# Kernel tuning notes

Measured on AMD Instinct MI355X. Metric: run time of the kernel, lower is better.

Reference implementation:

```python
import jax, jax.numpy as jnp
import numpy as np

H = 1.0  # RBF bandwidth (init kwarg h)


def setup_inputs() -> dict:
    key = jax.random.key(0)
    k1, k2 = jax.random.split(key)
    x = jax.random.normal(k1, (8192, 512), dtype=jnp.float32)
    x1 = jax.random.normal(k2, (8192, 512), dtype=jnp.float32)
    return {"x": x, "x1": x1}


def reference(x, x1):
    # exp(-||x_i - x1_j||^2 / h), computed via the GEMM trick to avoid the
    # O(N*M*D) broadcast intermediate the original torch code materializes.
    x_sq = jnp.sum(x * x, axis=-1, keepdims=True)          # [N, 1]
    x1_sq = jnp.sum(x1 * x1, axis=-1)                       # [M]
    cross = jnp.einsum('nd,md->nm', x, x1)                  # [N, M]
    d = jnp.maximum(x_sq + x1_sq[None, :] - 2.0 * cross, 0.0)
    return jnp.exp(-d / H)
```

## Files before the change

### kernel.cpp

```cpp
#include <hip/hip_runtime.h>
#include <stdint.h>
#include <stddef.h>


#define NROWS 8192
#define DIMK  512
#define BM    128
#define BN    128
#define BKB   128
#define KT    (DIMK / BKB)

typedef __bf16 bf16x8 __attribute__((ext_vector_type(8)));
typedef int    i32x8  __attribute__((ext_vector_type(8)));
typedef float  f32x4  __attribute__((ext_vector_type(4)));

#define AS1 __attribute__((address_space(1)))
#define AS3 __attribute__((address_space(3)))

__device__ __forceinline__ uint32_t f2bf(float f) {
    uint32_t u = __float_as_uint(f);
    return (u + 0x7FFFu + ((u >> 16) & 1u)) >> 16;
}

__device__ __forceinline__ uint32_t pk_fp8x4(float a, float b, float c, float d) {
    int w = __builtin_amdgcn_cvt_pk_fp8_f32(a, b, 0, false);
    w     = __builtin_amdgcn_cvt_pk_fp8_f32(c, d, w, true);
    return (uint32_t)w;
}

__global__ __launch_bounds__(256) void precast_fp8(
    const float* __restrict__ x, const float* __restrict__ x1,
    uint8_t* __restrict__ xf, uint8_t* __restrict__ x1f,
    float* __restrict__ xsq, float* __restrict__ x1sq)
{
    const int w    = threadIdx.x >> 6;
    const int lane = threadIdx.x & 63;
    const int row  = blockIdx.x * 4 + w;
    const float* src;
    uint8_t* dstb;
    float* dsts;
    if (blockIdx.y == 0) { src = x  + (size_t)row * DIMK; dstb = xf  + (size_t)row * DIMK; dsts = xsq  + row; }
    else                 { src = x1 + (size_t)row * DIMK; dstb = x1f + (size_t)row * DIMK; dsts = x1sq + row; }

    float4 v0 = ((const float4*)src)[lane * 2];
    float4 v1 = ((const float4*)src)[lane * 2 + 1];
    float s = v0.x * v0.x + v0.y * v0.y + v0.z * v0.z + v0.w * v0.w
            + v1.x * v1.x + v1.y * v1.y + v1.z * v1.z + v1.w * v1.w;

    uint2 p;
    p.x = pk_fp8x4(v0.x, v0.y, v0.z, v0.w);
    p.y = pk_fp8x4(v1.x, v1.y, v1.z, v1.w);
    ((uint2*)dstb)[lane] = p;

    #pragma unroll
    for (int off = 32; off > 0; off >>= 1) s += __shfl_down(s, off);
    if (lane == 0) *dsts = s;
}

__global__ __launch_bounds__(256) void norms_only(
    const float* __restrict__ x, const float* __restrict__ x1,
    float* __restrict__ xsq, float* __restrict__ x1sq)
{
    const int row = blockIdx.x;
    const float* src = (blockIdx.y == 0) ? x + (size_t)row * DIMK : x1 + (size_t)row * DIMK;
    float* dsts      = (blockIdx.y == 0) ? xsq + row : x1sq + row;
    const int t = threadIdx.x;
    float2 v = ((const float2*)src)[t];
    float s = v.x * v.x + v.y * v.y;
    #pragma unroll
    for (int off = 32; off > 0; off >>= 1) s += __shfl_down(s, off);
    __shared__ float red[4];
    if ((t & 63) == 0) red[t >> 6] = s;
    __syncthreads();
    if (t == 0) *dsts = red[0] + red[1] + red[2] + red[3];
}

__global__ __launch_bounds__(256, 3) void rbf_mfma_mxfp8(
    const uint8_t* __restrict__ Xf, const uint8_t* __restrict__ X1f,
    const float* __restrict__ xsq, const float* __restrict__ x1sq,
    float* __restrict__ out)
{
    __shared__ uint8_t As[BM * BKB];
    __shared__ uint8_t Bs[BN * BKB];

    const int t    = threadIdx.x;
    const int bm   = blockIdx.x;
    const int bn   = blockIdx.y;
    const int lane = t & 63;
    const int w    = t >> 6;
    const int wm   = w >> 1;
    const int wn   = w & 1;

    const int srow = t >> 3;
    const int scol = (t & 7) * 16;
    const uint8_t* gA = Xf  + (size_t)(bm * BM + srow) * DIMK + scol;
    const uint8_t* gB = X1f + (size_t)(bn * BN + srow) * DIMK + scol;
    uint8_t* lA = &As[t * 16];
    uint8_t* lB = &Bs[t * 16];

    f32x4 acc[4][4];
    #pragma unroll
    for (int i = 0; i < 4; ++i)
        #pragma unroll
        for (int j = 0; j < 4; ++j)
            acc[i][j] = f32x4{0.f, 0.f, 0.f, 0.f};

    const int lrow = lane & 15;
    const int kq   = (lane >> 4) * 32;
    int aoff[4], boff[4];
    #pragma unroll
    for (int i = 0; i < 4; ++i) {
        aoff[i] = (wm * 64 + i * 16 + lrow) * BKB + kq;
        boff[i] = (wn * 64 + i * 16 + lrow) * BKB + kq;
    }

    #pragma unroll 1
    for (int kt = 0; kt < KT; ++kt) {
        const uint8_t* ga = gA + kt * BKB;
        const uint8_t* gb = gB + kt * BKB;
        #pragma unroll
        for (int c = 0; c < 4; ++c) {
            __builtin_amdgcn_global_load_lds((AS1 void*)(ga + (size_t)c * 32 * DIMK),
                                             (AS3 void*)(lA + c * 4096), 16, 0, 0);
            __builtin_amdgcn_global_load_lds((AS1 void*)(gb + (size_t)c * 32 * DIMK),
                                             (AS3 void*)(lB + c * 4096), 16, 0, 0);
        }
        __syncthreads();

        i32x8 af[4], bg[4];
        #pragma unroll
        for (int i = 0; i < 4; ++i) af[i] = *(const i32x8*)&As[aoff[i]];
        #pragma unroll
        for (int i = 0; i < 4; ++i) bg[i] = *(const i32x8*)&Bs[boff[i]];
        #pragma unroll
        for (int i = 0; i < 4; ++i)
            #pragma unroll
            for (int j = 0; j < 4; ++j)
                acc[i][j] = __builtin_amdgcn_mfma_scale_f32_16x16x128_f8f6f4(
                    af[i], bg[j], acc[i][j],
                    0, 0,
                    0, 0x7F7F7F7F,
                    0, 0x7F7F7F7F);
        if (kt + 1 < KT) __syncthreads();
    }

    const int row0 = bm * BM + wm * 64 + (lane >> 4) * 4;
    const int col0 = bn * BN + wn * 64 + lrow;
    float xs[4][4], x1s[4];
    #pragma unroll
    for (int tm = 0; tm < 4; ++tm)
        #pragma unroll
        for (int r = 0; r < 4; ++r) xs[tm][r] = xsq[row0 + tm * 16 + r];
    #pragma unroll
    for (int tn = 0; tn < 4; ++tn) x1s[tn] = x1sq[col0 + tn * 16];

    #pragma unroll
    for (int tm = 0; tm < 4; ++tm)
        #pragma unroll
        for (int tn = 0; tn < 4; ++tn)
            #pragma unroll
            for (int r = 0; r < 4; ++r) {
                const int row = row0 + tm * 16 + r;
                const int col = col0 + tn * 16;
                float d = xs[tm][r] + x1s[tn] - 2.0f * acc[tm][tn][r];
                d = fmaxf(d, 0.0f);
                __builtin_nontemporal_store(__expf(-d), &out[(size_t)row * NROWS + col]);
            }
}

__global__ __launch_bounds__(256) void rbf_mfma_inline(
    const float* __restrict__ X, const float* __restrict__ X1,
    const float* __restrict__ xsq, const float* __restrict__ x1sq,
    float* __restrict__ out)
{
    __shared__ uint16_t As[BM * 32];
    __shared__ uint16_t Bs[BN * 32];

    const int t    = threadIdx.x;
    const int bm   = blockIdx.x;
    const int bn   = blockIdx.y;
    const int lane = t & 63;
    const int w    = t >> 6;
    const int wm   = w >> 1;
    const int wn   = w & 1;

    f32x4 acc[4][4];
    #pragma unroll
    for (int i = 0; i < 4; ++i)
        #pragma unroll
        for (int j = 0; j < 4; ++j)
            acc[i][j] = f32x4{0.f, 0.f, 0.f, 0.f};

    const int lrow = lane & 15;
    const int kq   = (lane >> 4) * 8;
    int aoff[4], boff[4];
    #pragma unroll
    for (int i = 0; i < 4; ++i) {
        aoff[i] = (wm * 64 + i * 16 + lrow) * 32 + kq;
        boff[i] = (wn * 64 + i * 16 + lrow) * 32 + kq;
    }

    #pragma unroll 1
    for (int kt = 0; kt < DIMK / 32; ++kt) {
        #pragma unroll
        for (int i = 0; i < 4; ++i) {
            const int g   = t + i * 256;
            const int row = g >> 3;
            const int c4  = (g & 7) * 4;
            float4 va = *(const float4*)&X [(size_t)(bm * BM + row) * DIMK + kt * 32 + c4];
            float4 vb = *(const float4*)&X1[(size_t)(bn * BN + row) * DIMK + kt * 32 + c4];
            uint2 pa, pb;
            pa.x = f2bf(va.x) | (f2bf(va.y) << 16);
            pa.y = f2bf(va.z) | (f2bf(va.w) << 16);
            pb.x = f2bf(vb.x) | (f2bf(vb.y) << 16);
            pb.y = f2bf(vb.z) | (f2bf(vb.w) << 16);
            *(uint2*)&As[g * 4] = pa;
            *(uint2*)&Bs[g * 4] = pb;
        }
        __syncthreads();

        bf16x8 af[4], bg[4];
        #pragma unroll
        for (int i = 0; i < 4; ++i) af[i] = *(const bf16x8*)&As[aoff[i]];
        #pragma unroll
        for (int i = 0; i < 4; ++i) bg[i] = *(const bf16x8*)&Bs[boff[i]];
        #pragma unroll
        for (int i = 0; i < 4; ++i)
            #pragma unroll
            for (int j = 0; j < 4; ++j)
                acc[i][j] = __builtin_amdgcn_mfma_f32_16x16x32_bf16(af[i], bg[j], acc[i][j], 0, 0, 0);
        __syncthreads();
    }

    const int row0 = bm * BM + wm * 64 + (lane >> 4) * 4;
    const int col0 = bn * BN + wn * 64 + lrow;
    float xs[4][4], x1s[4];
    #pragma unroll
    for (int tm = 0; tm < 4; ++tm)
        #pragma unroll
        for (int r = 0; r < 4; ++r) xs[tm][r] = xsq[row0 + tm * 16 + r];
    #pragma unroll
    for (int tn = 0; tn < 4; ++tn) x1s[tn] = x1sq[col0 + tn * 16];

    #pragma unroll
    for (int tm = 0; tm < 4; ++tm)
        #pragma unroll
        for (int tn = 0; tn < 4; ++tn)
            #pragma unroll
            for (int r = 0; r < 4; ++r) {
                const int row = row0 + tm * 16 + r;
                const int col = col0 + tn * 16;
                float d = xs[tm][r] + x1s[tn] - 2.0f * acc[tm][tn][r];
                d = fmaxf(d, 0.0f);
                out[(size_t)row * NROWS + col] = __expf(-d);
            }
}

extern "C" void kernel_launch(void* const* d_in, const int* in_sizes, int n_in,
                              void* d_out, int out_size, void* d_ws, size_t ws_size,
                              hipStream_t stream)
{
    const float* x  = (const float*)d_in[0];
    const float* x1 = (const float*)d_in[1];
    float* out = (float*)d_out;

    const size_t f8_bytes  = (size_t)NROWS * DIMK;
    const size_t need_full = 2 * f8_bytes + 2 * (size_t)NROWS * sizeof(float);

    dim3 gridG(NROWS / BM, NROWS / BN);

    if (ws_size >= need_full) {
        uint8_t* xf   = (uint8_t*)d_ws;
        uint8_t* x1f  = xf + f8_bytes;
        float*   xsq  = (float*)((char*)d_ws + 2 * f8_bytes);
        float*   x1sq = xsq + NROWS;
        precast_fp8<<<dim3(NROWS / 4, 2), 256, 0, stream>>>(x, x1, xf, x1f, xsq, x1sq);
        rbf_mfma_mxfp8<<<gridG, 256, 0, stream>>>(xf, x1f, xsq, x1sq, out);
    } else {
        float* xsq  = (float*)d_ws;
        float* x1sq = xsq + NROWS;
        norms_only<<<dim3(NROWS, 2), 256, 0, stream>>>(x, x1, xsq, x1sq);
        rbf_mfma_inline<<<gridG, 256, 0, stream>>>(x, x1, xsq, x1sq, out);
    }
}
```

Baseline: 319.2 us.

## Swizzle LDS layout for fp8 MFMA tiles and hoist norm loads

Applies an XOR swizzle to the 16-byte chunks written into shared memory and reads fragments through two matching 16-byte loads, to reduce LDS bank conflicts on the MFMA operand reads. It also moves the squared-norm loads before the main loop so they overlap with the GEMM, fully unrolls the K loop, and drops the occupancy hint from the launch bounds. Output stores change from nontemporal to plain stores, which may affect cache behaviour on the large 256MB output write.

```diff
diff --git a/kernel.cpp b/kernel.cpp
--- a/kernel.cpp
+++ b/kernel.cpp
@@ -12,6 +12,7 @@
 
 typedef __bf16 bf16x8 __attribute__((ext_vector_type(8)));
 typedef int    i32x8  __attribute__((ext_vector_type(8)));
+typedef int    i32x4  __attribute__((ext_vector_type(4)));
 typedef float  f32x4  __attribute__((ext_vector_type(4)));
 
 #define AS1 __attribute__((address_space(1)))
@@ -26,6 +27,15 @@
     int w = __builtin_amdgcn_cvt_pk_fp8_f32(a, b, 0, false);
     w     = __builtin_amdgcn_cvt_pk_fp8_f32(c, d, w, true);
     return (uint32_t)w;
+}
+
+__device__ __forceinline__ i32x8 ld_frag(const uint8_t* base, int c_lo, int c_hi) {
+    i32x4 lo = *(const i32x4*)(base + c_lo);
+    i32x4 hi = *(const i32x4*)(base + c_hi);
+    i32x8 r;
+    r[0] = lo[0]; r[1] = lo[1]; r[2] = lo[2]; r[3] = lo[3];
+    r[4] = hi[0]; r[5] = hi[1]; r[6] = hi[2]; r[7] = hi[3];
+    return r;
 }
 
 __global__ __launch_bounds__(256) void precast_fp8(
@@ -75,7 +85,7 @@
     if (t == 0) *dsts = red[0] + red[1] + red[2] + red[3];
 }
 
-__global__ __launch_bounds__(256, 3) void rbf_mfma_mxfp8(
+__global__ __launch_bounds__(256) void rbf_mfma_mxfp8(
     const uint8_t* __restrict__ Xf, const uint8_t* __restrict__ X1f,
     const float* __restrict__ xsq, const float* __restrict__ x1sq,
     float* __restrict__ out)
@@ -91,13 +101,24 @@
     const int wm   = w >> 1;
     const int wn   = w & 1;
 
-    const int srow = t >> 3;
-    const int scol = (t & 7) * 16;
-    const uint8_t* gA = Xf  + (size_t)(bm * BM + srow) * DIMK + scol;
-    const uint8_t* gB = X1f + (size_t)(bn * BN + srow) * DIMK + scol;
+    const int srow   = t >> 3;
+    const int schunk = (t & 7) ^ (srow & 7);
+    const uint8_t* gA = Xf  + (size_t)(bm * BM + srow) * DIMK + schunk * 16;
+    const uint8_t* gB = X1f + (size_t)(bn * BN + srow) * DIMK + schunk * 16;
     uint8_t* lA = &As[t * 16];
     uint8_t* lB = &Bs[t * 16];
 
+    const int lrow = lane & 15;
+    const int row0 = bm * BM + wm * 64 + (lane >> 4) * 4;
+    const int col0 = bn * BN + wn * 64 + lrow;
+    float xs[4][4], x1s[4];
+    #pragma unroll
+    for (int tm = 0; tm < 4; ++tm)
+        #pragma unroll
+        for (int r = 0; r < 4; ++r) xs[tm][r] = xsq[row0 + tm * 16 + r];
+    #pragma unroll
+    for (int tn = 0; tn < 4; ++tn) x1s[tn] = x1sq[col0 + tn * 16];
+
     f32x4 acc[4][4];
     #pragma unroll
     for (int i = 0; i < 4; ++i)
@@ -105,16 +126,15 @@
         for (int j = 0; j < 4; ++j)
             acc[i][j] = f32x4{0.f, 0.f, 0.f, 0.f};
 
-    const int lrow = lane & 15;
-    const int kq   = (lane >> 4) * 32;
-    int aoff[4], boff[4];
-    #pragma unroll
-    for (int i = 0; i < 4; ++i) {
-        aoff[i] = (wm * 64 + i * 16 + lrow) * BKB + kq;
-        boff[i] = (wn * 64 + i * 16 + lrow) * BKB + kq;
-    }
-
-    #pragma unroll 1
+    const int q    = lane >> 4;
+    const int s    = lrow & 7;
+    const int c_lo = ((2 * q)     ^ s) * 16;
+    const int c_hi = ((2 * q + 1) ^ s) * 16;
+    int roff[4];
+    #pragma unroll
+    for (int i = 0; i < 4; ++i) roff[i] = (i * 16 + lrow) * BKB;
+
+    #pragma unroll
     for (int kt = 0; kt < KT; ++kt) {
         const uint8_t* ga = gA + kt * BKB;
         const uint8_t* gb = gB + kt * BKB;
@@ -129,9 +149,11 @@
 
         i32x8 af[4], bg[4];
         #pragma unroll
-        for (int i = 0; i < 4; ++i) af[i] = *(const i32x8*)&As[aoff[i]];
-        #pragma unroll
-        for (int i = 0; i < 4; ++i) bg[i] = *(const i32x8*)&Bs[boff[i]];
+        for (int i = 0; i < 4; ++i)
+            af[i] = ld_frag(&As[wm * 64 * BKB + roff[i]], c_lo, c_hi);
+        #pragma unroll
+        for (int i = 0; i < 4; ++i)
+            bg[i] = ld_frag(&Bs[wn * 64 * BKB + roff[i]], c_lo, c_hi);
         #pragma unroll
         for (int i = 0; i < 4; ++i)
             #pragma unroll
@@ -141,18 +163,8 @@
                     0, 0,
                     0, 0x7F7F7F7F,
                     0, 0x7F7F7F7F);
-        if (kt + 1 < KT) __syncthreads();
-    }
-
-    const int row0 = bm * BM + wm * 64 + (lane >> 4) * 4;
-    const int col0 = bn * BN + wn * 64 + lrow;
-    float xs[4][4], x1s[4];
-    #pragma unroll
-    for (int tm = 0; tm < 4; ++tm)
-        #pragma unroll
-        for (int r = 0; r < 4; ++r) xs[tm][r] = xsq[row0 + tm * 16 + r];
-    #pragma unroll
-    for (int tn = 0; tn < 4; ++tn) x1s[tn] = x1sq[col0 + tn * 16];
+        __syncthreads();
+    }
 
     #pragma unroll
     for (int tm = 0; tm < 4; ++tm)
@@ -164,7 +176,7 @@
                 const int col = col0 + tn * 16;
                 float d = xs[tm][r] + x1s[tn] - 2.0f * acc[tm][tn][r];
                 d = fmaxf(d, 0.0f);
-                __builtin_nontemporal_store(__expf(-d), &out[(size_t)row * NROWS + col]);
+                out[(size_t)row * NROWS + col] = __expf(-d);
             }
 }
 
```

Result: faster. 308.2 us (-3.5%).
